# Optimization experiments

Hardware: AMD Instinct MI355X
Metric: run time of the kernel (lower is better)

The kernel has to match this reference:

```python
import jax, jax.numpy as jnp
import numpy as np

B, K = 32768, 9  # batch, sudoku size


def setup_inputs() -> dict:
    key = jax.random.key(0)
    k1, = jax.random.split(key, 1)
    # binary possibility masks, as the module expects 0/1 sudoku tensors
    sudoku = (jax.random.uniform(k1, (B, K, K, K)) > 0.5).astype(jnp.float32)
    return {
        "sudoku": sudoku,
        "recursion_mask": jnp.zeros((B, K, K, K), jnp.float32),
        "recursion_index": jnp.ones((B, 1, 1, 1), jnp.float32),
        "conv_w": jnp.ones((1, K, 1, 1), jnp.float32),
        "conv_b": jnp.zeros((1,), jnp.float32),
    }


def reference(sudoku, recursion_mask, recursion_index, conv_w, conv_b):
    b = sudoku.shape[0]

    def conv1x1(x):  # channel-sum 1x1 conv: [b,K,K,K] -> [b,1,K,K]
        return jnp.sum(x * conv_w.reshape(1, K, 1, 1), axis=1, keepdims=True) + conv_b.reshape(1, 1, 1, 1)

    # number of candidates in each cell, minus 1, negated; empty cells pushed to -K
    nic = jax.nn.relu(conv1x1(sudoku) - 1.0)
    mask0 = jnp.clip(1.0 - jnp.abs(nic), 0.0, 1.0) * (-K)  # NNCompare(nic, 0) * -K
    nic = mask0 - nic  # [b,1,K,K]

    # MaxPool2d(K) + MaxUnpool2d(K): one-hot at the (first) argmax cell of the board
    idx = jnp.argmax(nic.reshape(b, K * K), axis=-1)
    current_cell_mask = jax.nn.one_hot(idx, K * K, dtype=sudoku.dtype).reshape(b, 1, K, K)

    # SudokuSelectOneVariant: per-cell MaxPool1d(K)+unpool over the number channel
    s = jnp.transpose(sudoku, (0, 3, 2, 1)).reshape(b, K * K, K)  # [b, cells, numbers]
    mval = jnp.max(s, axis=-1)
    midx = jnp.argmax(s, axis=-1)
    filt = jax.nn.one_hot(midx, K, dtype=sudoku.dtype) * mval[..., None]
    filt = jnp.transpose(filt.reshape(b, K, K, K), (0, 3, 2, 1))  # back to [b,K,K,K]
    one_variant = filt * current_cell_mask

    # mark all other candidates in the chosen cell, remove them from sudoku
    cell_mask = jnp.clip(conv1x1(one_variant), 0.0, 1.0)
    one_recursion_mask = sudoku * cell_mask * (1.0 - one_variant)  # NNAnd(.., NNNot(..))
    recursion_mask = jnp.maximum(recursion_mask, recursion_index * one_recursion_mask)
    recursion_mask = jnp.maximum(recursion_mask, (recursion_index - 1.0) * one_variant)
    sudoku_out = sudoku * (1.0 - one_recursion_mask)
    return sudoku_out, recursion_mask, recursion_index + 1.0
```

## Files before the change

kernel.cpp:

```cpp
#include <hip/hip_runtime.h>

#define BDIM   256
#define BPB    4
#define KK     9
#define CELLS  81
#define BOARD  729
#define CHUNK  (BPB * BOARD)

__global__ __launch_bounds__(BDIM) void sudoku_iter_kernel(
    const float* __restrict__ sudoku,
    const float* __restrict__ rmask,
    const float* __restrict__ rindex,
    const float* __restrict__ conv_w,
    const float* __restrict__ conv_b,
    float* __restrict__ out,
    int Btot)
{
    __shared__ float lds_s[CHUNK];
    __shared__ int   meta_e[BPB];
    __shared__ int   meta_cell[BPB];
    __shared__ float meta_m[BPB];
    __shared__ float meta_cms[BPB];
    __shared__ float meta_ri[BPB];

    const int tid   = threadIdx.x;
    const int block = blockIdx.x;
    const size_t base = (size_t)block * CHUNK;

    float wreg[KK];
    #pragma unroll
    for (int n = 0; n < KK; ++n) wreg[n] = conv_w[n];
    const float bias = conv_b[0];
    const float cmp  = fminf(fmaxf(bias, 0.f), 1.f);

    const float4* gsrc = (const float4*)(sudoku + base);
    float4* lds4 = (float4*)lds_s;
    #pragma unroll
    for (int i = 0; i < 3; ++i) {
        int g = tid + i * BDIM;
        if (g < CHUNK / 4) lds4[g] = gsrc[g];
    }
    __syncthreads();

    {
        const int wave = tid >> 6;
        const int lane = tid & 63;
        const float* bs = lds_s + wave * BOARD;

        float v0; int i0;
        {
            const int cell = lane;
            float cnt = bias;
            #pragma unroll
            for (int n = 0; n < KK; ++n) cnt += bs[n * CELLS + cell] * wreg[n];
            float nic = fmaxf(cnt - 1.f, 0.f);
            float m0  = fminf(fmaxf(1.f - nic, 0.f), 1.f) * (-(float)KK);
            v0 = m0 - nic; i0 = cell;
        }
        if (lane < CELLS - 64) {
            const int cell = lane + 64;
            float cnt = bias;
            #pragma unroll
            for (int n = 0; n < KK; ++n) cnt += bs[n * CELLS + cell] * wreg[n];
            float nic = fmaxf(cnt - 1.f, 0.f);
            float m0  = fminf(fmaxf(1.f - nic, 0.f), 1.f) * (-(float)KK);
            float v1 = m0 - nic;
            if (v1 > v0) { v0 = v1; i0 = cell; }
        }
        #pragma unroll
        for (int off = 32; off > 0; off >>= 1) {
            float ov = __shfl_xor(v0, off, 64);
            int   oi = __shfl_xor(i0, off, 64);
            if (ov > v0 || (ov == v0 && oi < i0)) { v0 = ov; i0 = oi; }
        }
        if (lane == 0) {
            const int cell = i0;
            float m = bs[cell]; int nstar = 0;
            #pragma unroll
            for (int n = 1; n < KK; ++n) {
                float v = bs[n * CELLS + cell];
                if (v > m) { m = v; nstar = n; }
            }
            meta_e[wave]    = nstar * CELLS + cell;
            meta_cell[wave] = cell;
            meta_m[wave]    = m;
            meta_cms[wave]  = fminf(fmaxf(m * wreg[nstar] + bias, 0.f), 1.f);
            meta_ri[wave]   = rindex[block * BPB + wave];
        }
    }
    __syncthreads();

    const float4* grm4   = (const float4*)(rmask + base);
    float4*       gout_s = (float4*)(out + base);
    float4*       gout_r = (float4*)(out + (size_t)Btot * BOARD + base);

    #pragma unroll
    for (int i = 0; i < 3; ++i) {
        int g = tid + i * BDIM;
        if (g < CHUNK / 4) {
            float4 s4 = lds4[g];
            float4 r4 = grm4[g];
            float so[4], ro[4];
            const float* sp = (const float*)&s4;
            const float* rp = (const float*)&r4;
            #pragma unroll
            for (int j = 0; j < 4; ++j) {
                int f = 4 * g + j;
                int bl = (f >= 1458) ? (f >= 2187 ? 3 : 2) : (f >= 729 ? 1 : 0);
                int e = f - bl * BOARD;
                int cell = e % CELLS;
                float s  = sp[j];
                float rm = rp[j];
                float m   = meta_m[bl];
                float riv = meta_ri[bl];
                float ov  = (e == meta_e[bl]) ? m : 0.f;
                float cm  = (cell == meta_cell[bl]) ? meta_cms[bl] : cmp;
                float orm = s * cm * (1.f - ov);
                float rmo = fmaxf(rm, riv * orm);
                rmo = fmaxf(rmo, (riv - 1.f) * ov);
                so[j] = s * (1.f - orm);
                ro[j] = rmo;
            }
            gout_s[g] = make_float4(so[0], so[1], so[2], so[3]);
            gout_r[g] = make_float4(ro[0], ro[1], ro[2], ro[3]);
        }
    }

    if (tid < BPB) {
        out[(size_t)Btot * BOARD * 2 + (size_t)block * BPB + tid] = meta_ri[tid] + 1.f;
    }
}

extern "C" void kernel_launch(void* const* d_in, const int* in_sizes, int n_in,
                              void* d_out, int out_size, void* d_ws, size_t ws_size,
                              hipStream_t stream) {
    const float* sudoku = (const float*)d_in[0];
    const float* rmask  = (const float*)d_in[1];
    const float* rindex = (const float*)d_in[2];
    const float* conv_w = (const float*)d_in[3];
    const float* conv_b = (const float*)d_in[4];
    float* out = (float*)d_out;

    const int Btot = in_sizes[2];
    const int nblocks = Btot / BPB;

    sudoku_iter_kernel<<<nblocks, BDIM, 0, stream>>>(
        sudoku, rmask, rindex, conv_w, conv_b, out, Btot);
}
```

Before: 330.3 us.

## Make each wave own one board, drop block barriers, keep data in registers

```diff
diff --git a/kernel.cpp b/kernel.cpp
--- a/kernel.cpp
+++ b/kernel.cpp
@@ -1,11 +1,14 @@
 #include <hip/hip_runtime.h>
 
+typedef float v4f __attribute__((ext_vector_type(4)));
+
 #define BDIM   256
-#define BPB    4
 #define KK     9
 #define CELLS  81
 #define BOARD  729
+#define BPB    4
 #define CHUNK  (BPB * BOARD)
+#define LDSW   736
 
 __global__ __launch_bounds__(BDIM) void sudoku_iter_kernel(
     const float* __restrict__ sudoku,
@@ -16,16 +19,45 @@
     float* __restrict__ out,
     int Btot)
 {
-    __shared__ float lds_s[CHUNK];
-    __shared__ int   meta_e[BPB];
-    __shared__ int   meta_cell[BPB];
-    __shared__ float meta_m[BPB];
-    __shared__ float meta_cms[BPB];
-    __shared__ float meta_ri[BPB];
+    __shared__ float lds_s[BPB * LDSW];
 
-    const int tid   = threadIdx.x;
-    const int block = blockIdx.x;
-    const size_t base = (size_t)block * CHUNK;
+    const int tid  = threadIdx.x;
+    const int wave = tid >> 6;
+    const int lane = tid & 63;
+    const int blk  = blockIdx.x;
+    const size_t base = (size_t)blk * CHUNK;
+
+    const int fstart = wave * BOARD;
+    const int g_lo   = (fstart + 3) >> 2;
+    const int g_hi   = (fstart + BOARD) >> 2;
+    const int h      = 4 * g_lo - fstart;
+    const int t      = fstart + BOARD - 4 * g_hi;
+    const int n4     = g_hi - g_lo;
+
+    const v4f* gs4 = (const v4f*)(sudoku + base);
+    const v4f* gr4 = (const v4f*)(rmask  + base);
+    v4f s4[3], r4[3];
+    bool act[3];
+    #pragma unroll
+    for (int i = 0; i < 3; ++i) {
+        int k2 = lane + 64 * i;
+        act[i] = (k2 < n4);
+        if (act[i]) s4[i] = gs4[g_lo + k2];
+    }
+    const bool hasH = (lane < h);
+    const bool hasT = (lane >= 8) && (lane < 8 + t);
+    const int  eH   = lane;
+    const int  eT   = BOARD - t + (lane - 8);
+    float sh = 0.f, st = 0.f, rh = 0.f, rt = 0.f;
+    if (hasH) sh = sudoku[base + fstart + eH];
+    if (hasT) st = sudoku[base + fstart + eT];
+    #pragma unroll
+    for (int i = 0; i < 3; ++i) {
+        if (act[i]) r4[i] = gr4[g_lo + lane + 64 * i];
+    }
+    if (hasH) rh = rmask[base + fstart + eH];
+    if (hasT) rt = rmask[base + fstart + eT];
+    float ri0 = (lane == 0) ? rindex[blk * BPB + wave] : 0.f;
 
     float wreg[KK];
     #pragma unroll
@@ -33,101 +65,108 @@
     const float bias = conv_b[0];
     const float cmp  = fminf(fmaxf(bias, 0.f), 1.f);
 
-    const float4* gsrc = (const float4*)(sudoku + base);
-    float4* lds4 = (float4*)lds_s;
+    float* bs  = lds_s + wave * LDSW + (4 - h);
+    v4f*   bs4 = (v4f*)(lds_s + wave * LDSW + 4);
     #pragma unroll
     for (int i = 0; i < 3; ++i) {
-        int g = tid + i * BDIM;
-        if (g < CHUNK / 4) lds4[g] = gsrc[g];
+        if (act[i]) bs4[lane + 64 * i] = s4[i];
     }
-    __syncthreads();
+    if (hasH) bs[eH] = sh;
+    if (hasT) bs[eT] = st;
 
+    float v0; int i0;
     {
-        const int wave = tid >> 6;
-        const int lane = tid & 63;
-        const float* bs = lds_s + wave * BOARD;
+        const int cell = lane;
+        float cnt = bias;
+        #pragma unroll
+        for (int n = 0; n < KK; ++n) cnt += bs[n * CELLS + cell] * wreg[n];
+        float nic = fmaxf(cnt - 1.f, 0.f);
+        float m0  = fminf(fmaxf(1.f - nic, 0.f), 1.f) * (-(float)KK);
+        v0 = m0 - nic; i0 = cell;
+    }
+    if (lane < CELLS - 64) {
+        const int cell = lane + 64;
+        float cnt = bias;
+        #pragma unroll
+        for (int n = 0; n < KK; ++n) cnt += bs[n * CELLS + cell] * wreg[n];
+        float nic = fmaxf(cnt - 1.f, 0.f);
+        float m0  = fminf(fmaxf(1.f - nic, 0.f), 1.f) * (-(float)KK);
+        float v1 = m0 - nic;
+        if (v1 > v0) { v0 = v1; i0 = cell; }
+    }
+    #pragma unroll
+    for (int off = 32; off > 0; off >>= 1) {
+        float ov = __shfl_xor(v0, off, 64);
+        int   oi = __shfl_xor(i0, off, 64);
+        if (ov > v0 || (ov == v0 && oi < i0)) { v0 = ov; i0 = oi; }
+    }
+    float m = 0.f, cms = 0.f; int es = 0, cellstar = 0;
+    if (lane == 0) {
+        cellstar = i0;
+        m = bs[cellstar]; int nstar = 0;
+        #pragma unroll
+        for (int n = 1; n < KK; ++n) {
+            float v = bs[n * CELLS + cellstar];
+            if (v > m) { m = v; nstar = n; }
+        }
+        es  = nstar * CELLS + cellstar;
+        cms = fminf(fmaxf(m * wreg[nstar] + bias, 0.f), 1.f);
+    }
+    m        = __shfl(m, 0, 64);
+    cms      = __shfl(cms, 0, 64);
+    es       = __shfl(es, 0, 64);
+    cellstar = __shfl(cellstar, 0, 64);
+    const float ri = __shfl(ri0, 0, 64);
 
-        float v0; int i0;
-        {
-            const int cell = lane;
-            float cnt = bias;
-            #pragma unroll
-            for (int n = 0; n < KK; ++n) cnt += bs[n * CELLS + cell] * wreg[n];
-            float nic = fmaxf(cnt - 1.f, 0.f);
-            float m0  = fminf(fmaxf(1.f - nic, 0.f), 1.f) * (-(float)KK);
-            v0 = m0 - nic; i0 = cell;
-        }
-        if (lane < CELLS - 64) {
-            const int cell = lane + 64;
-            float cnt = bias;
-            #pragma unroll
-            for (int n = 0; n < KK; ++n) cnt += bs[n * CELLS + cell] * wreg[n];
-            float nic = fmaxf(cnt - 1.f, 0.f);
-            float m0  = fminf(fmaxf(1.f - nic, 0.f), 1.f) * (-(float)KK);
-            float v1 = m0 - nic;
-            if (v1 > v0) { v0 = v1; i0 = cell; }
-        }
-        #pragma unroll
-        for (int off = 32; off > 0; off >>= 1) {
-            float ov = __shfl_xor(v0, off, 64);
-            int   oi = __shfl_xor(i0, off, 64);
-            if (ov > v0 || (ov == v0 && oi < i0)) { v0 = ov; i0 = oi; }
-        }
-        if (lane == 0) {
-            const int cell = i0;
-            float m = bs[cell]; int nstar = 0;
-            #pragma unroll
-            for (int n = 1; n < KK; ++n) {
-                float v = bs[n * CELLS + cell];
-                if (v > m) { m = v; nstar = n; }
-            }
-            meta_e[wave]    = nstar * CELLS + cell;
-            meta_cell[wave] = cell;
-            meta_m[wave]    = m;
-            meta_cms[wave]  = fminf(fmaxf(m * wreg[nstar] + bias, 0.f), 1.f);
-            meta_ri[wave]   = rindex[block * BPB + wave];
-        }
-    }
-    __syncthreads();
-
-    const float4* grm4   = (const float4*)(rmask + base);
-    float4*       gout_s = (float4*)(out + base);
-    float4*       gout_r = (float4*)(out + (size_t)Btot * BOARD + base);
+    v4f* os4 = (v4f*)(out + base);
+    v4f* or4 = (v4f*)(out + (size_t)Btot * BOARD + base);
+    const int ebase = h + 4 * lane;
+    const int cbase = ebase % CELLS;
+    const int iadd[3] = {0, 13, 26};
 
     #pragma unroll
     for (int i = 0; i < 3; ++i) {
-        int g = tid + i * BDIM;
-        if (g < CHUNK / 4) {
-            float4 s4 = lds4[g];
-            float4 r4 = grm4[g];
+        if (act[i]) {
             float so[4], ro[4];
-            const float* sp = (const float*)&s4;
-            const float* rp = (const float*)&r4;
+            const float* sp = (const float*)&s4[i];
+            const float* rp = (const float*)&r4[i];
             #pragma unroll
             for (int j = 0; j < 4; ++j) {
-                int f = 4 * g + j;
-                int bl = (f >= 1458) ? (f >= 2187 ? 3 : 2) : (f >= 729 ? 1 : 0);
-                int e = f - bl * BOARD;
-                int cell = e % CELLS;
+                int e = ebase + 256 * i + j;
+                int cell = cbase + iadd[i] + j;
+                if (cell >= CELLS) cell -= CELLS;
                 float s  = sp[j];
                 float rm = rp[j];
-                float m   = meta_m[bl];
-                float riv = meta_ri[bl];
-                float ov  = (e == meta_e[bl]) ? m : 0.f;
-                float cm  = (cell == meta_cell[bl]) ? meta_cms[bl] : cmp;
+                float ov  = (e == es) ? m : 0.f;
+                float cm  = (cell == cellstar) ? cms : cmp;
                 float orm = s * cm * (1.f - ov);
-                float rmo = fmaxf(rm, riv * orm);
-                rmo = fmaxf(rmo, (riv - 1.f) * ov);
+                float rmo = fmaxf(rm, ri * orm);
+                rmo = fmaxf(rmo, (ri - 1.f) * ov);
                 so[j] = s * (1.f - orm);
                 ro[j] = rmo;
             }
-            gout_s[g] = make_float4(so[0], so[1], so[2], so[3]);
-            gout_r[g] = make_float4(ro[0], ro[1], ro[2], ro[3]);
+            v4f sv; sv.x = so[0]; sv.y = so[1]; sv.z = so[2]; sv.w = so[3];
+            v4f rv; rv.x = ro[0]; rv.y = ro[1]; rv.z = ro[2]; rv.w = ro[3];
+            __builtin_nontemporal_store(sv, &os4[g_lo + lane + 64 * i]);
+            __builtin_nontemporal_store(rv, &or4[g_lo + lane + 64 * i]);
         }
     }
+    if (hasH | hasT) {
+        int   e  = hasH ? eH : eT;
+        float s  = hasH ? sh : st;
+        float rm = hasH ? rh : rt;
+        int cell = (e >= 648) ? (e - 648) : e;
+        float ov  = (e == es) ? m : 0.f;
+        float cm  = (cell == cellstar) ? cms : cmp;
+        float orm = s * cm * (1.f - ov);
+        float rmo = fmaxf(rm, ri * orm);
+        rmo = fmaxf(rmo, (ri - 1.f) * ov);
+        __builtin_nontemporal_store(s * (1.f - orm), out + base + fstart + e);
+        __builtin_nontemporal_store(rmo, out + (size_t)Btot * BOARD + base + fstart + e);
+    }
 
-    if (tid < BPB) {
-        out[(size_t)Btot * BOARD * 2 + (size_t)block * BPB + tid] = meta_ri[tid] + 1.f;
+    if (lane == 0) {
+        out[(size_t)Btot * BOARD * 2 + (size_t)blk * BPB + wave] = ri + 1.f;
     }
 }
 
```

New measurement: 336.4 us. Within noise of the previous version (+1.9%).

## Split into select and apply kernels with per-board metadata in workspace

Applied to the files above, without the earlier changes.

```diff
diff --git a/kernel.cpp b/kernel.cpp
--- a/kernel.cpp
+++ b/kernel.cpp
@@ -1,133 +1,173 @@
 #include <hip/hip_runtime.h>
 
-#define BDIM   256
-#define BPB    4
-#define KK     9
-#define CELLS  81
-#define BOARD  729
-#define CHUNK  (BPB * BOARD)
+typedef float v4f __attribute__((ext_vector_type(4)));
 
-__global__ __launch_bounds__(BDIM) void sudoku_iter_kernel(
+#define KK      9
+#define CELLS   81
+#define BOARD   729
+#define B1      8
+#define SEL_V4  (B1 * BOARD / 4)
+#define AP_V4   1024
+
+__global__ __launch_bounds__(256) void select_kernel(
     const float* __restrict__ sudoku,
-    const float* __restrict__ rmask,
     const float* __restrict__ rindex,
     const float* __restrict__ conv_w,
     const float* __restrict__ conv_b,
-    float* __restrict__ out,
+    v4f*   __restrict__ meta,
+    float* __restrict__ out_ri,
     int Btot)
 {
-    __shared__ float lds_s[CHUNK];
-    __shared__ int   meta_e[BPB];
-    __shared__ int   meta_cell[BPB];
-    __shared__ float meta_m[BPB];
-    __shared__ float meta_cms[BPB];
-    __shared__ float meta_ri[BPB];
+    __shared__ float sb[B1 * BOARD];
 
-    const int tid   = threadIdx.x;
-    const int block = blockIdx.x;
-    const size_t base = (size_t)block * CHUNK;
+    const int tid = threadIdx.x;
+    const int blk = blockIdx.x;
+    const size_t base = (size_t)blk * (B1 * BOARD);
+
+    const v4f* g4 = (const v4f*)(sudoku + base);
+    v4f* s4 = (v4f*)sb;
+    #pragma unroll
+    for (int k = 0; k < 6; ++k) {
+        int idx = tid + k * 256;
+        if (idx < SEL_V4) s4[idx] = g4[idx];
+    }
 
     float wreg[KK];
     #pragma unroll
     for (int n = 0; n < KK; ++n) wreg[n] = conv_w[n];
     const float bias = conv_b[0];
+
+    __syncthreads();
+
+    const int g = tid >> 5;
+    const int l = tid & 31;
+    const float* bs = sb + g * BOARD;
+    const int board = blk * B1 + g;
+
+    float v0; int i0;
+    {
+        const int cell = l;
+        float cnt = bias;
+        #pragma unroll
+        for (int n = 0; n < KK; ++n) cnt += bs[n * CELLS + cell] * wreg[n];
+        float nic = fmaxf(cnt - 1.f, 0.f);
+        float m0  = fminf(fmaxf(1.f - nic, 0.f), 1.f) * (-(float)KK);
+        v0 = m0 - nic; i0 = cell;
+    }
+    {
+        const int cell = l + 32;
+        float cnt = bias;
+        #pragma unroll
+        for (int n = 0; n < KK; ++n) cnt += bs[n * CELLS + cell] * wreg[n];
+        float nic = fmaxf(cnt - 1.f, 0.f);
+        float m0  = fminf(fmaxf(1.f - nic, 0.f), 1.f) * (-(float)KK);
+        float v1 = m0 - nic;
+        if (v1 > v0) { v0 = v1; i0 = cell; }
+    }
+    if (l < CELLS - 64) {
+        const int cell = l + 64;
+        float cnt = bias;
+        #pragma unroll
+        for (int n = 0; n < KK; ++n) cnt += bs[n * CELLS + cell] * wreg[n];
+        float nic = fmaxf(cnt - 1.f, 0.f);
+        float m0  = fminf(fmaxf(1.f - nic, 0.f), 1.f) * (-(float)KK);
+        float v1 = m0 - nic;
+        if (v1 > v0) { v0 = v1; i0 = cell; }
+    }
+    #pragma unroll
+    for (int off = 16; off > 0; off >>= 1) {
+        float ov = __shfl_xor(v0, off, 64);
+        int   oi = __shfl_xor(i0, off, 64);
+        if (ov > v0 || (ov == v0 && oi < i0)) { v0 = ov; i0 = oi; }
+    }
+    const int cellstar = i0;
+    float m = bs[cellstar]; int nstar = 0;
+    #pragma unroll
+    for (int n = 1; n < KK; ++n) {
+        float v = bs[n * CELLS + cellstar];
+        if (v > m) { m = v; nstar = n; }
+    }
+    if (l == 0) {
+        const float ri  = rindex[board];
+        const float cms = fminf(fmaxf(m * wreg[nstar] + bias, 0.f), 1.f);
+        const int   es  = nstar * CELLS + cellstar;
+        v4f mt;
+        ((int*)&mt)[0] = es | (cellstar << 16);
+        mt.y = m; mt.z = cms; mt.w = ri;
+        meta[board]   = mt;
+        out_ri[board] = ri + 1.f;
+    }
+}
+
+__global__ __launch_bounds__(256) void apply_kernel(
+    const float* __restrict__ sudoku,
+    const float* __restrict__ rmask,
+    const float* __restrict__ conv_b,
+    const v4f* __restrict__ meta,
+    float* __restrict__ out,
+    int Btot)
+{
+    const float bias = conv_b[0];
     const float cmp  = fminf(fmaxf(bias, 0.f), 1.f);
 
-    const float4* gsrc = (const float4*)(sudoku + base);
-    float4* lds4 = (float4*)lds_s;
-    #pragma unroll
-    for (int i = 0; i < 3; ++i) {
-        int g = tid + i * BDIM;
-        if (g < CHUNK / 4) lds4[g] = gsrc[g];
-    }
-    __syncthreads();
-
-    {
-        const int wave = tid >> 6;
-        const int lane = tid & 63;
-        const float* bs = lds_s + wave * BOARD;
-
-        float v0; int i0;
-        {
-            const int cell = lane;
-            float cnt = bias;
-            #pragma unroll
-            for (int n = 0; n < KK; ++n) cnt += bs[n * CELLS + cell] * wreg[n];
-            float nic = fmaxf(cnt - 1.f, 0.f);
-            float m0  = fminf(fmaxf(1.f - nic, 0.f), 1.f) * (-(float)KK);
-            v0 = m0 - nic; i0 = cell;
-        }
-        if (lane < CELLS - 64) {
-            const int cell = lane + 64;
-            float cnt = bias;
-            #pragma unroll
-            for (int n = 0; n < KK; ++n) cnt += bs[n * CELLS + cell] * wreg[n];
-            float nic = fmaxf(cnt - 1.f, 0.f);
-            float m0  = fminf(fmaxf(1.f - nic, 0.f), 1.f) * (-(float)KK);
-            float v1 = m0 - nic;
-            if (v1 > v0) { v0 = v1; i0 = cell; }
-        }
-        #pragma unroll
-        for (int off = 32; off > 0; off >>= 1) {
-            float ov = __shfl_xor(v0, off, 64);
-            int   oi = __shfl_xor(i0, off, 64);
-            if (ov > v0 || (ov == v0 && oi < i0)) { v0 = ov; i0 = oi; }
-        }
-        if (lane == 0) {
-            const int cell = i0;
-            float m = bs[cell]; int nstar = 0;
-            #pragma unroll
-            for (int n = 1; n < KK; ++n) {
-                float v = bs[n * CELLS + cell];
-                if (v > m) { m = v; nstar = n; }
-            }
-            meta_e[wave]    = nstar * CELLS + cell;
-            meta_cell[wave] = cell;
-            meta_m[wave]    = m;
-            meta_cms[wave]  = fminf(fmaxf(m * wreg[nstar] + bias, 0.f), 1.f);
-            meta_ri[wave]   = rindex[block * BPB + wave];
-        }
-    }
-    __syncthreads();
-
-    const float4* grm4   = (const float4*)(rmask + base);
-    float4*       gout_s = (float4*)(out + base);
-    float4*       gout_r = (float4*)(out + (size_t)Btot * BOARD + base);
+    const int tid = threadIdx.x;
+    const size_t tbase = (size_t)blockIdx.x * AP_V4;
+    const v4f* gs = (const v4f*)sudoku;
+    const v4f* gr = (const v4f*)rmask;
+    v4f* os = (v4f*)out;
+    v4f* orr = (v4f*)(out + (size_t)Btot * BOARD);
 
     #pragma unroll
-    for (int i = 0; i < 3; ++i) {
-        int g = tid + i * BDIM;
-        if (g < CHUNK / 4) {
-            float4 s4 = lds4[g];
-            float4 r4 = grm4[g];
-            float so[4], ro[4];
-            const float* sp = (const float*)&s4;
-            const float* rp = (const float*)&r4;
-            #pragma unroll
-            for (int j = 0; j < 4; ++j) {
-                int f = 4 * g + j;
-                int bl = (f >= 1458) ? (f >= 2187 ? 3 : 2) : (f >= 729 ? 1 : 0);
-                int e = f - bl * BOARD;
-                int cell = e % CELLS;
-                float s  = sp[j];
-                float rm = rp[j];
-                float m   = meta_m[bl];
-                float riv = meta_ri[bl];
-                float ov  = (e == meta_e[bl]) ? m : 0.f;
-                float cm  = (cell == meta_cell[bl]) ? meta_cms[bl] : cmp;
-                float orm = s * cm * (1.f - ov);
-                float rmo = fmaxf(rm, riv * orm);
-                rmo = fmaxf(rmo, (riv - 1.f) * ov);
-                so[j] = s * (1.f - orm);
-                ro[j] = rmo;
+    for (int k = 0; k < 4; ++k) {
+        const unsigned gv = (unsigned)tbase + k * 256 + tid;
+        v4f s = gs[gv];
+        v4f r = gr[gv];
+
+        const unsigned f0 = gv * 4u;
+        unsigned b  = f0 / 729u;
+        int e0 = (int)(f0 - b * 729u);
+        v4f mt = meta[b];
+        int   p1   = ((const int*)&mt)[0];
+        int   es1  = p1 & 0xFFFF;
+        int   cs1  = p1 >> 16;
+        float m1   = mt.y, cms1 = mt.z, ri1 = mt.w;
+
+        int   es2 = es1, cs2 = cs1;
+        float m2 = m1, cms2 = cms1, ri2 = ri1;
+        if (e0 >= BOARD - 3) {
+            unsigned b1 = b + 1; if (b1 >= (unsigned)Btot) b1 = b;
+            v4f mt2 = meta[b1];
+            int p2 = ((const int*)&mt2)[0];
+            es2 = p2 & 0xFFFF; cs2 = p2 >> 16;
+            m2 = mt2.y; cms2 = mt2.z; ri2 = mt2.w;
+        }
+
+        const int cell0 = e0 % 81;
+        float so[4], ro[4];
+        #pragma unroll
+        for (int j = 0; j < 4; ++j) {
+            int e = e0 + j;
+            int cell = cell0 + j; if (cell >= CELLS) cell -= CELLS;
+            int   es = es1, cs = cs1;
+            float mm = m1, cms = cms1, ri = ri1;
+            if (e >= BOARD) {
+                e -= BOARD; cell = e;
+                es = es2; cs = cs2; mm = m2; cms = cms2; ri = ri2;
             }
-            gout_s[g] = make_float4(so[0], so[1], so[2], so[3]);
-            gout_r[g] = make_float4(ro[0], ro[1], ro[2], ro[3]);
+            float sj = s[j];
+            float rj = r[j];
+            float ov  = (e == es) ? mm : 0.f;
+            float cm  = (cell == cs) ? cms : cmp;
+            float orm = sj * cm * (1.f - ov);
+            float rmo = fmaxf(rj, ri * orm);
+            rmo = fmaxf(rmo, (ri - 1.f) * ov);
+            so[j] = sj * (1.f - orm);
+            ro[j] = rmo;
         }
-    }
-
-    if (tid < BPB) {
-        out[(size_t)Btot * BOARD * 2 + (size_t)block * BPB + tid] = meta_ri[tid] + 1.f;
+        v4f sv; sv.x = so[0]; sv.y = so[1]; sv.z = so[2]; sv.w = so[3];
+        v4f rv; rv.x = ro[0]; rv.y = ro[1]; rv.z = ro[2]; rv.w = ro[3];
+        __builtin_nontemporal_store(sv, &os[gv]);
+        __builtin_nontemporal_store(rv, &orr[gv]);
     }
 }
 
@@ -142,8 +182,14 @@
     float* out = (float*)d_out;
 
     const int Btot = in_sizes[2];
-    const int nblocks = Btot / BPB;
+    v4f* meta = (v4f*)d_ws;
 
-    sudoku_iter_kernel<<<nblocks, BDIM, 0, stream>>>(
-        sudoku, rmask, rindex, conv_w, conv_b, out, Btot);
+    const int nb1 = Btot / B1;
+    select_kernel<<<nb1, 256, 0, stream>>>(
+        sudoku, rindex, conv_w, conv_b, meta,
+        out + (size_t)Btot * BOARD * 2, Btot);
+
+    const int nb2 = (Btot * BOARD / 4) / AP_V4;
+    apply_kernel<<<nb2, 256, 0, stream>>>(
+        sudoku, rmask, conv_b, meta, out, Btot);
 }
```

Result: no change. 332.8 us (+0.8%).

## Load sudoku and recursion mask via global_load_lds, use nontemporal stores

Applied to the files above, without the earlier changes.

```diff
diff --git a/kernel.cpp b/kernel.cpp
--- a/kernel.cpp
+++ b/kernel.cpp
@@ -1,11 +1,21 @@
 #include <hip/hip_runtime.h>
 
+typedef float v4f __attribute__((ext_vector_type(4)));
+
 #define BDIM   256
-#define BPB    4
 #define KK     9
 #define CELLS  81
 #define BOARD  729
+#define BPB    4
 #define CHUNK  (BPB * BOARD)
+#define NV4    (CHUNK / 4)
+
+__device__ __forceinline__ void ld_g2l_16(const float* g, float* l) {
+    __builtin_amdgcn_global_load_lds(
+        (const __attribute__((address_space(1))) unsigned int*)g,
+        (__attribute__((address_space(3))) unsigned int*)l,
+        16, 0, 0);
+}
 
 __global__ __launch_bounds__(BDIM) void sudoku_iter_kernel(
     const float* __restrict__ sudoku,
@@ -16,16 +26,30 @@
     float* __restrict__ out,
     int Btot)
 {
-    __shared__ float lds_s[CHUNK];
+    __shared__ __align__(16) float sA[CHUNK];
+    __shared__ __align__(16) float sR[CHUNK];
     __shared__ int   meta_e[BPB];
     __shared__ int   meta_cell[BPB];
     __shared__ float meta_m[BPB];
     __shared__ float meta_cms[BPB];
     __shared__ float meta_ri[BPB];
 
-    const int tid   = threadIdx.x;
-    const int block = blockIdx.x;
-    const size_t base = (size_t)block * CHUNK;
+    const int tid = threadIdx.x;
+    const int blk = blockIdx.x;
+    const size_t base = (size_t)blk * CHUNK;
+
+    const float* gA = sudoku + base;
+    const float* gR = rmask  + base;
+    #pragma unroll
+    for (int j = 0; j < 3; ++j) {
+        int idx = j * BDIM + tid;
+        if (idx < NV4) ld_g2l_16(gA + idx * 4, &sA[idx * 4]);
+    }
+    #pragma unroll
+    for (int j = 0; j < 3; ++j) {
+        int idx = j * BDIM + tid;
+        if (idx < NV4) ld_g2l_16(gR + idx * 4, &sR[idx * 4]);
+    }
 
     float wreg[KK];
     #pragma unroll
@@ -33,19 +57,12 @@
     const float bias = conv_b[0];
     const float cmp  = fminf(fmaxf(bias, 0.f), 1.f);
 
-    const float4* gsrc = (const float4*)(sudoku + base);
-    float4* lds4 = (float4*)lds_s;
-    #pragma unroll
-    for (int i = 0; i < 3; ++i) {
-        int g = tid + i * BDIM;
-        if (g < CHUNK / 4) lds4[g] = gsrc[g];
-    }
     __syncthreads();
 
     {
         const int wave = tid >> 6;
         const int lane = tid & 63;
-        const float* bs = lds_s + wave * BOARD;
+        const float* bs = sA + wave * BOARD;
 
         float v0; int i0;
         {
@@ -73,61 +90,68 @@
             int   oi = __shfl_xor(i0, off, 64);
             if (ov > v0 || (ov == v0 && oi < i0)) { v0 = ov; i0 = oi; }
         }
+        const int cellstar = i0;
+        float m = bs[cellstar]; int nstar = 0;
+        #pragma unroll
+        for (int n = 1; n < KK; ++n) {
+            float v = bs[n * CELLS + cellstar];
+            if (v > m) { m = v; nstar = n; }
+        }
         if (lane == 0) {
-            const int cell = i0;
-            float m = bs[cell]; int nstar = 0;
-            #pragma unroll
-            for (int n = 1; n < KK; ++n) {
-                float v = bs[n * CELLS + cell];
-                if (v > m) { m = v; nstar = n; }
-            }
-            meta_e[wave]    = nstar * CELLS + cell;
-            meta_cell[wave] = cell;
+            meta_e[wave]    = nstar * CELLS + cellstar;
+            meta_cell[wave] = cellstar;
             meta_m[wave]    = m;
             meta_cms[wave]  = fminf(fmaxf(m * wreg[nstar] + bias, 0.f), 1.f);
-            meta_ri[wave]   = rindex[block * BPB + wave];
+            meta_ri[wave]   = rindex[blk * BPB + wave];
         }
     }
     __syncthreads();
 
-    const float4* grm4   = (const float4*)(rmask + base);
-    float4*       gout_s = (float4*)(out + base);
-    float4*       gout_r = (float4*)(out + (size_t)Btot * BOARD + base);
+    v4f* os4 = (v4f*)(out + base);
+    v4f* or4 = (v4f*)(out + (size_t)Btot * BOARD + base);
+    const v4f* sA4 = (const v4f*)sA;
+    const v4f* sR4 = (const v4f*)sR;
+
+    const int c0 = (4 * tid) % 81;
+    const int iadd[3] = {0, 52, 23};
 
     #pragma unroll
     for (int i = 0; i < 3; ++i) {
         int g = tid + i * BDIM;
-        if (g < CHUNK / 4) {
-            float4 s4 = lds4[g];
-            float4 r4 = grm4[g];
+        if (g < NV4) {
+            v4f s4 = sA4[g];
+            v4f r4 = sR4[g];
             float so[4], ro[4];
             const float* sp = (const float*)&s4;
             const float* rp = (const float*)&r4;
             #pragma unroll
             for (int j = 0; j < 4; ++j) {
                 int f = 4 * g + j;
-                int bl = (f >= 1458) ? (f >= 2187 ? 3 : 2) : (f >= 729 ? 1 : 0);
-                int e = f - bl * BOARD;
-                int cell = e % CELLS;
+                int blj = (f >= 1458) ? (f >= 2187 ? 3 : 2) : (f >= 729 ? 1 : 0);
+                int e = f - blj * BOARD;
+                int cell = c0 + iadd[i] + j;
+                if (cell >= CELLS) cell -= CELLS;
                 float s  = sp[j];
                 float rm = rp[j];
-                float m   = meta_m[bl];
-                float riv = meta_ri[bl];
-                float ov  = (e == meta_e[bl]) ? m : 0.f;
-                float cm  = (cell == meta_cell[bl]) ? meta_cms[bl] : cmp;
+                float mm  = meta_m[blj];
+                float riv = meta_ri[blj];
+                float ov  = (e == meta_e[blj]) ? mm : 0.f;
+                float cm  = (cell == meta_cell[blj]) ? meta_cms[blj] : cmp;
                 float orm = s * cm * (1.f - ov);
                 float rmo = fmaxf(rm, riv * orm);
                 rmo = fmaxf(rmo, (riv - 1.f) * ov);
                 so[j] = s * (1.f - orm);
                 ro[j] = rmo;
             }
-            gout_s[g] = make_float4(so[0], so[1], so[2], so[3]);
-            gout_r[g] = make_float4(ro[0], ro[1], ro[2], ro[3]);
+            v4f sv; sv.x = so[0]; sv.y = so[1]; sv.z = so[2]; sv.w = so[3];
+            v4f rv; rv.x = ro[0]; rv.y = ro[1]; rv.z = ro[2]; rv.w = ro[3];
+            __builtin_nontemporal_store(sv, &os4[g]);
+            __builtin_nontemporal_store(rv, &or4[g]);
         }
     }
 
     if (tid < BPB) {
-        out[(size_t)Btot * BOARD * 2 + (size_t)block * BPB + tid] = meta_ri[tid] + 1.f;
+        out[(size_t)Btot * BOARD * 2 + (size_t)blk * BPB + tid] = meta_ri[tid] + 1.f;
     }
 }
 
```

New measurement: 334.1 us. No clear change (+1.2%).
